# Kernel optimization log

Hardware: AMD Instinct MI355X
Metric: run time of the kernel (lower is better)

The kernel has to match this reference:

```python
import jax, jax.numpy as jnp
import numpy as np

H = 16  # n_heads

def setup_inputs() -> dict:
    key = jax.random.key(0)
    ks = jax.random.split(key, 11)
    B, L, D = 2, 2048, 1024
    w = 1.0 / np.sqrt(D).astype(np.float32)
    return {
        "query": jax.random.normal(ks[0], (B, L, D), jnp.float32),
        "key":   jax.random.normal(ks[1], (B, L, D), jnp.float32),
        "value": jax.random.normal(ks[2], (B, L, D), jnp.float32),
        "Wq": jax.random.normal(ks[3], (D, D), jnp.float32) * w,
        "bq": jax.random.normal(ks[4], (D,), jnp.float32) * 0.01,
        "Wk": jax.random.normal(ks[5], (D, D), jnp.float32) * w,
        "bk": jax.random.normal(ks[6], (D,), jnp.float32) * 0.01,
        "Wv": jax.random.normal(ks[7], (D, D), jnp.float32) * w,
        "bv": jax.random.normal(ks[8], (D,), jnp.float32) * 0.01,
        "Wo": jax.random.normal(ks[9], (D, D), jnp.float32) * w,
        "bo": jax.random.normal(ks[10], (D,), jnp.float32) * 0.01,
        "masksize": 256,
    }

def reference(query, key, value, Wq, bq, Wk, bk, Wv, bv, Wo, bo, masksize):
    B, L, D = query.shape
    d_k = D // H
    scale = 1.0 / np.sqrt(d_k).astype(np.float32)

    def proj(x, W, b):
        # nn.Linear: x @ W.T + b, then [B,L,H,d_k] -> [B,H,L,d_k]
        return (x @ W.T + b).reshape(B, L, H, d_k).transpose(0, 2, 1, 3)

    q = proj(query, Wq, bq)
    k = proj(key, Wk, bk)
    v = proj(value, Wv, bv)

    # Sliding-window float mask (faithful to original: a 0/1 FLOAT tensor is
    # passed as attn_mask to SDPA, so it is ADDED to scores, not -inf-masked).
    half = masksize // 2
    i = jnp.arange(L)[:, None]
    j = jnp.arange(L)[None, :]
    band = (jnp.abs(i - j) <= half).astype(q.dtype)  # [L, L]

    scores = jnp.einsum('bhqd,bhkd->bhqk', q, k) * scale + band  # [B,H,L,L]
    attn = jax.nn.softmax(scores, axis=-1)
    out = jnp.einsum('bhqk,bhkd->bhqd', attn, v)  # [B,H,L,d_k]
    out = out.transpose(0, 2, 1, 3).reshape(B, L, D)
    return out @ Wo.T + bo
```

## Files before the change

### kernel.cpp

```cpp
#include <hip/hip_runtime.h>
#include <hip/hip_bf16.h>

#define Hh 16
#define Ll 2048
#define Dd 1024
#define DK 64
#define Mm 4096
#define Kk 1024
#define Nn 1024

typedef short bf16x8 __attribute__((ext_vector_type(8)));
typedef float f32x4 __attribute__((ext_vector_type(4)));

static __device__ __forceinline__ unsigned short f2bf(float f) {
    union { __hip_bfloat16 b; unsigned short u; } cv;
    cv.b = __float2bfloat16(f);
    return cv.u;
}

static __device__ __forceinline__ unsigned packtr(float a, float b) {
    return __builtin_amdgcn_perm(__builtin_bit_cast(unsigned, b),
                                 __builtin_bit_cast(unsigned, a), 0x07060302u);
}

static __device__ __forceinline__ float fexp2(float x) {
    return __builtin_amdgcn_exp2f(x);
}

static __device__ __forceinline__ void glds16(const ushort* g, ushort* l) {
    __builtin_amdgcn_global_load_lds((const __attribute__((address_space(1))) unsigned int*)g,
                                     (__attribute__((address_space(3))) unsigned int*)l,
                                     16, 0, 0);
}

__global__ __launch_bounds__(256) void cast_all(
    const float* __restrict__ q, const float* __restrict__ k, const float* __restrict__ v,
    const float* __restrict__ wq, const float* __restrict__ wk, const float* __restrict__ wv,
    const float* __restrict__ wo,
    ushort* __restrict__ qb, ushort* __restrict__ kb, ushort* __restrict__ vb,
    ushort* __restrict__ wqb, ushort* __restrict__ wkb, ushort* __restrict__ wvb,
    ushort* __restrict__ wob) {
    const int bx = blockIdx.x;
    const float4* s; ushort4* d; int base;
    if      (bx <  4096) { s = (const float4*)q;  d = (ushort4*)qb;  base = 0; }
    else if (bx <  8192) { s = (const float4*)k;  d = (ushort4*)kb;  base = 4096; }
    else if (bx < 12288) { s = (const float4*)v;  d = (ushort4*)vb;  base = 8192; }
    else if (bx < 13312) { s = (const float4*)wq; d = (ushort4*)wqb; base = 12288; }
    else if (bx < 14336) { s = (const float4*)wk; d = (ushort4*)wkb; base = 13312; }
    else if (bx < 15360) { s = (const float4*)wv; d = (ushort4*)wvb; base = 14336; }
    else                 { s = (const float4*)wo; d = (ushort4*)wob; base = 15360; }
    const int i = (bx - base) * 256 + threadIdx.x;
    float4 vv = s[i];
    ushort4 o;
    o.x = f2bf(vv.x); o.y = f2bf(vv.y); o.z = f2bf(vv.z); o.w = f2bf(vv.w);
    d[i] = o;
}

__global__ __launch_bounds__(256) void gemm_qkv(
    const ushort* __restrict__ A0, const ushort* __restrict__ A1, const ushort* __restrict__ A2,
    const ushort* __restrict__ W0, const ushort* __restrict__ W1, const ushort* __restrict__ W2,
    const float* __restrict__ b0, const float* __restrict__ b1, const float* __restrict__ b2,
    ushort* __restrict__ O0, ushort* __restrict__ O1, ushort* __restrict__ OVt) {
    __shared__ __align__(16) ushort SM[2 * 128 * 32];
    ushort* As = SM;
    ushort* Bs = SM + 4096;

    const int fl = blockIdx.x;
    const int xcd = fl & 7, bcoli = (fl >> 3) & 7, slot = fl >> 6;
    const int g = slot * 8 + xcd;
    const int z = g >> 5;
    const int browi = g & 31;

    const ushort* A = (z == 0) ? A0 : (z == 1) ? A1 : A2;
    const ushort* W = (z == 0) ? W0 : (z == 1) ? W1 : W2;
    const float* bias = (z == 0) ? b0 : (z == 1) ? b1 : b2;

    const int t = threadIdx.x;
    const int wave = t >> 6, lane = t & 63;
    const int quad = lane >> 4, l15 = lane & 15;
    const int brow = browi * 128, bcol = bcoli * 128;
    const int wr = (wave >> 1) * 64, wc = (wave & 1) * 64;
    const int gr = wave * 16 + (lane >> 2);
    const int gc = (lane & 3) * 8;

    f32x4 acc[4][4] = {};

    for (int k0 = 0; k0 < Kk; k0 += 32) {
        __syncthreads();
        glds16(A + (size_t)(brow + gr) * Kk + k0 + gc,      As + wave * 512);
        glds16(A + (size_t)(brow + 64 + gr) * Kk + k0 + gc, As + 2048 + wave * 512);
        glds16(W + (size_t)(bcol + gr) * Kk + k0 + gc,      Bs + wave * 512);
        glds16(W + (size_t)(bcol + 64 + gr) * Kk + k0 + gc, Bs + 2048 + wave * 512);
        __syncthreads();

        bf16x8 af[4], bfr[4];
#pragma unroll
        for (int i = 0; i < 4; i++)
            af[i] = *(const bf16x8*)(As + (wr + i * 16 + l15) * 32 + quad * 8);
#pragma unroll
        for (int j = 0; j < 4; j++)
            bfr[j] = *(const bf16x8*)(Bs + (wc + j * 16 + l15) * 32 + quad * 8);
#pragma unroll
        for (int i = 0; i < 4; i++)
#pragma unroll
            for (int j = 0; j < 4; j++)
                acc[i][j] = __builtin_amdgcn_mfma_f32_16x16x32_bf16(af[i], bfr[j], acc[i][j], 0, 0, 0);
    }

    if (z < 2) {
        ushort* Out = (z == 0) ? O0 : O1;
        const float oscl = (z == 0) ? 0.18033688f : 1.0f;
        const int b = brow >> 11;
        const int lbase = (brow & 2047) + wr;
        const int h = (bcol + wc) >> 6;
        ushort* T = SM + wave * 1280;
        __syncthreads();
#pragma unroll
        for (int i = 0; i < 4; i++) {
#pragma unroll
            for (int j = 0; j < 4; j++) {
                const float bv = bias[bcol + wc + j * 16 + l15];
#pragma unroll
                for (int r = 0; r < 4; r++)
                    T[(quad * 4 + r) * 80 + j * 16 + l15] = f2bf((acc[i][j][r] + bv) * oscl);
            }
            const int r8 = lane >> 3, c8 = lane & 7;
#pragma unroll
            for (int pass = 0; pass < 2; pass++) {
                const uint4 val = *(const uint4*)(T + (pass * 8 + r8) * 80 + c8 * 8);
                const int l = lbase + i * 16 + pass * 8 + r8;
                *(uint4*)(Out + ((size_t)(b * Hh + h) * Ll + l) * DK + c8 * 8) = val;
            }
        }
    } else {
        ushort* T = SM;
        const int b = brow >> 11;
        const int lbase = brow & 2047;
        const int npr = (wave & 1) * 16 + l15;
#pragma unroll
        for (int j = 0; j < 4; j++) {
            __syncthreads();
            const float bv = bias[bcol + wc + j * 16 + l15];
#pragma unroll
            for (int i = 0; i < 4; i++)
#pragma unroll
                for (int r = 0; r < 4; r++) {
                    const int m = wr + i * 16 + quad * 4 + r;
                    T[npr * 136 + m] = f2bf(acc[i][j][r] + bv);
                }
            __syncthreads();
#pragma unroll
            for (int cc = 0; cc < 2; cc++) {
                const int idx = t + cc * 256;
                const int ni = idx >> 4;
                const int ms = idx & 15;
                const int n = bcol + (ni >> 4) * 64 + j * 16 + (ni & 15);
                const int hh = n >> 6, dk = n & 63;
                uint4 val = *(const uint4*)(T + ni * 136 + ms * 8);
                *(uint4*)(OVt + ((size_t)(b * Hh + hh) * DK + dk) * Ll + lbase + ms * 8) = val;
            }
        }
    }
}

__global__ __launch_bounds__(256, 2) void attn_kernel(const ushort* __restrict__ Q,
                                                      const ushort* __restrict__ Kp,
                                                      const ushort* __restrict__ Vt,
                                                      ushort* __restrict__ Oout,
                                                      const int* __restrict__ masksize) {
    __shared__ __align__(16) ushort SM[32768];
    const int t = threadIdx.x;
    const int wave = t >> 6, lane = t & 63;
    const int quad = lane >> 4, l15 = lane & 15;
    const int bx = blockIdx.x;
    const int bh = bx & 31, qc = bx >> 5;
    const int q0w = qc * 128 + wave * 32;
    const int half = masksize[0] >> 1;
    const unsigned wid = (unsigned)(2 * half);

    const ushort* Qb = Q + (size_t)bh * (Ll * DK);
    const ushort* Kb = Kp + (size_t)bh * (Ll * DK);
    const ushort* Vb = Vt + (size_t)bh * (DK * Ll);

    const bf16x8 qA0 = *(const bf16x8*)(Qb + (size_t)(q0w + l15) * DK + quad * 8);
    const bf16x8 qA1 = *(const bf16x8*)(Qb + (size_t)(q0w + l15) * DK + 32 + quad * 8);
    const bf16x8 qB0 = *(const bf16x8*)(Qb + (size_t)(q0w + 16 + l15) * DK + quad * 8);
    const bf16x8 qB1 = *(const bf16x8*)(Qb + (size_t)(q0w + 16 + l15) * DK + 32 + quad * 8);

    const float C2IN  = (1.0f - 24.0f) * 1.44269504088896f;
    const float C2OUT = -24.0f * 1.44269504088896f;
    const float E1 = 2.718281828f;

    bf16x8 onesf;
#pragma unroll
    for (int j = 0; j < 8; j++) onesf[j] = (short)0x3F80;

    f32x4 OA0[4] = {}, OB0[4] = {}, OA1[4] = {}, OB1[4] = {};
    f32x4 SA0 = {}, SB0 = {}, SA1 = {}, SB1 = {};

    const int krow = lane >> 2;
    const int kcol8 = (((lane & 3) ^ ((lane >> 3) & 3)) * 8);
    const int qsw8 = (quad ^ ((l15 >> 1) & 3)) * 8;
    const int vd8 = lane >> 3;
    const int vgp = 2 * (lane & 7);

#define STAGE_J(J, BUF)                                                                    \
    do {                                                                                   \
        const int kt0_ = (J) * 64, kt1_ = 1024 + (J) * 64;                                 \
        if (wave < 2) {                                                                    \
            const int ktk_ = (wave == 0) ? kt0_ : kt1_;                                    \
            ushort* dst_ = SM + wave * 8192 + (BUF) * 4096;                                \
            _Pragma("unroll")                                                              \
            for (int c_ = 0; c_ < 4; c_++)                                                 \
                _Pragma("unroll")                                                          \
                for (int pan_ = 0; pan_ < 2; pan_++)                                       \
                    glds16(Kb + (size_t)(ktk_ + c_ * 16 + krow) * DK + pan_ * 32 + kcol8,  \
                           dst_ + pan_ * 2048 + c_ * 512);                                 \
        } else {                                                                           \
            const int ktv_ = (wave == 2) ? kt0_ : kt1_;                                    \
            ushort* dst_ = SM + 16384 + (wave - 2) * 8192 + (BUF) * 4096;                  \
            _Pragma("unroll")                                                              \
            for (int s_ = 0; s_ < 8; s_++) {                                               \
                const int d_ = s_ * 8 + vd8;                                               \
                glds16(Vb + (size_t)d_ * Ll + ktv_ + ((vgp ^ (d_ & 14)) * 4),              \
                       dst_ + s_ * 512);                                                   \
            }                                                                              \
        }                                                                                  \
    } while (0)

#define STREAM_BODY(KB, VB, KT, CV, OAx, OBx, SAx, SBx, UNIF)                              \
    _Pragma("unroll")                                                                      \
    for (int s = 0; s < 2; s++) {                                                          \
        const bf16x8 kf00 = *(const bf16x8*)((KB) + ((2 * s) * 16 + l15) * 32 + qsw8);     \
        const bf16x8 kf01 = *(const bf16x8*)((KB) + 2048 + ((2 * s) * 16 + l15) * 32 + qsw8); \
        const bf16x8 kf10 = *(const bf16x8*)((KB) + ((2 * s + 1) * 16 + l15) * 32 + qsw8); \
        const bf16x8 kf11 = *(const bf16x8*)((KB) + 2048 + ((2 * s + 1) * 16 + l15) * 32 + qsw8); \
        f32x4 zA0 = __builtin_amdgcn_mfma_f32_16x16x32_bf16(kf00, qA0, (CV), 0, 0, 0);     \
        zA0 = __builtin_amdgcn_mfma_f32_16x16x32_bf16(kf01, qA1, zA0, 0, 0, 0);            \
        f32x4 zA1 = __builtin_amdgcn_mfma_f32_16x16x32_bf16(kf10, qA0, (CV), 0, 0, 0);     \
        zA1 = __builtin_amdgcn_mfma_f32_16x16x32_bf16(kf11, qA1, zA1, 0, 0, 0);            \
        f32x4 zB0 = __builtin_amdgcn_mfma_f32_16x16x32_bf16(kf00, qB0, (CV), 0, 0, 0);     \
        zB0 = __builtin_amdgcn_mfma_f32_16x16x32_bf16(kf01, qB1, zB0, 0, 0, 0);            \
        f32x4 zB1 = __builtin_amdgcn_mfma_f32_16x16x32_bf16(kf10, qB0, (CV), 0, 0, 0);     \
        zB1 = __builtin_amdgcn_mfma_f32_16x16x32_bf16(kf11, qB1, zB1, 0, 0, 0);            \
        float pA[8], pB[8];                                                                \
        if (UNIF) {                                                                        \
            _Pragma("unroll")                                                              \
            for (int g = 0; g < 2; g++)                                                    \
                _Pragma("unroll")                                                          \
                for (int r = 0; r < 4; r++) {                                              \
                    pA[g * 4 + r] = fexp2(g ? zA1[r] : zA0[r]);                            \
                    pB[g * 4 + r] = fexp2(g ? zB1[r] : zB0[r]);                            \
                }                                                                          \
        } else {                                                                           \
            const int kb = (KT) + s * 32 + quad * 4 + half;                                \
            _Pragma("unroll")                                                              \
            for (int g = 0; g < 2; g++)                                                    \
                _Pragma("unroll")                                                          \
                for (int r = 0; r < 4; r++) {                                              \
                    const unsigned ttA = (unsigned)(kb + g * 16 + r - (q0w + l15));        \
                    const unsigned ttB = (unsigned)(kb + g * 16 + r - (q0w + 16 + l15));   \
                    pA[g * 4 + r] = fexp2(g ? zA1[r] : zA0[r]) * (ttA <= wid ? E1 : 1.0f); \
                    pB[g * 4 + r] = fexp2(g ? zB1[r] : zB0[r]) * (ttB <= wid ? E1 : 1.0f); \
                }                                                                          \
        }                                                                                  \
        bf16x8 pfA, pfB;                                                                   \
        ((unsigned*)&pfA)[0] = packtr(pA[0], pA[1]);                                       \
        ((unsigned*)&pfA)[1] = packtr(pA[2], pA[3]);                                       \
        ((unsigned*)&pfA)[2] = packtr(pA[4], pA[5]);                                       \
        ((unsigned*)&pfA)[3] = packtr(pA[6], pA[7]);                                       \
        ((unsigned*)&pfB)[0] = packtr(pB[0], pB[1]);                                       \
        ((unsigned*)&pfB)[1] = packtr(pB[2], pB[3]);                                       \
        ((unsigned*)&pfB)[2] = packtr(pB[4], pB[5]);                                       \
        ((unsigned*)&pfB)[3] = packtr(pB[6], pB[7]);                                       \
        SAx = __builtin_amdgcn_mfma_f32_16x16x32_bf16(pfA, onesf, SAx, 0, 0, 0);           \
        SBx = __builtin_amdgcn_mfma_f32_16x16x32_bf16(pfB, onesf, SBx, 0, 0, 0);           \
        _Pragma("unroll")                                                                  \
        for (int i = 0; i < 4; i++) {                                                      \
            const int bi = (i * 16 + l15) * 64;                                            \
            const int x14 = l15 & 14;                                                      \
            const ushort4 v1 = *(const ushort4*)((VB) + bi + (((s * 8 + quad) ^ x14) * 4)); \
            const ushort4 v2 = *(const ushort4*)((VB) + bi + (((s * 8 + 4 + quad) ^ x14) * 4)); \
            bf16x8 vc;                                                                     \
            *(ushort4*)&vc = v1;                                                           \
            *((ushort4*)&vc + 1) = v2;                                                     \
            OAx[i] = __builtin_amdgcn_mfma_f32_16x16x32_bf16(pfA, vc, OAx[i], 0, 0, 0);    \
            OBx[i] = __builtin_amdgcn_mfma_f32_16x16x32_bf16(pfB, vc, OBx[i], 0, 0, 0);    \
        }                                                                                  \
    }

    STAGE_J(0, 0);
    int cur = 0;
    const int qlo = q0w, qhi = q0w + 31;

    for (int j = 0; j < 16; ++j) {
        const int kt0 = j * 64, kt1 = 1024 + j * 64;
        __syncthreads();
        if (j < 15) STAGE_J(j + 1, cur ^ 1);

        const ushort* K0b = SM + cur * 4096;
        const ushort* K1b = SM + 8192 + cur * 4096;
        const ushort* V0b = SM + 16384 + cur * 4096;
        const ushort* V1b = SM + 24576 + cur * 4096;

        const bool allout0 = (kt0 + 63 < qlo - half) || (kt0 > qhi + half);
        const bool allin0  = (kt0 >= qhi - half) && (kt0 + 63 <= qlo + half);
        const bool allout1 = (kt1 + 63 < qlo - half) || (kt1 > qhi + half);
        const bool allin1  = (kt1 >= qhi - half) && (kt1 + 63 <= qlo + half);

        if ((allin0 || allout0) && (allin1 || allout1)) {
            const float c0 = allin0 ? C2IN : C2OUT;
            const float c1 = allin1 ? C2IN : C2OUT;
            const f32x4 cv0 = {c0, c0, c0, c0};
            const f32x4 cv1 = {c1, c1, c1, c1};
            STREAM_BODY(K0b, V0b, kt0, cv0, OA0, OB0, SA0, SB0, 1);
            STREAM_BODY(K1b, V1b, kt1, cv1, OA1, OB1, SA1, SB1, 1);
        } else {
            const f32x4 cvo = {C2OUT, C2OUT, C2OUT, C2OUT};
            STREAM_BODY(K0b, V0b, kt0, cvo, OA0, OB0, SA0, SB0, 0);
            STREAM_BODY(K1b, V1b, kt1, cvo, OA1, OB1, SA1, SB1, 0);
        }
        cur ^= 1;
    }
#undef STAGE_J
#undef STREAM_BODY

    float liA[4], liB[4];
#pragma unroll
    for (int r = 0; r < 4; r++) {
        liA[r] = 1.0f / (SA0[r] + SA1[r]);
        liB[r] = 1.0f / (SB0[r] + SB1[r]);
    }

    const int b = bh >> 4, h = bh & 15;
#pragma unroll
    for (int i = 0; i < 4; i++)
#pragma unroll
        for (int r = 0; r < 4; r++) {
            const int qa = q0w + quad * 4 + r;
            Oout[((size_t)b * Ll + qa) * Dd + h * DK + i * 16 + l15] =
                f2bf((OA0[i][r] + OA1[i][r]) * liA[r]);
            Oout[((size_t)b * Ll + qa + 16) * Dd + h * DK + i * 16 + l15] =
                f2bf((OB0[i][r] + OB1[i][r]) * liB[r]);
        }
}

__global__ __launch_bounds__(256) void gemm_o(const ushort* __restrict__ A,
                                              const ushort* __restrict__ W,
                                              const float* __restrict__ bias,
                                              float* __restrict__ Out) {
    __shared__ __align__(16) ushort As[64 * 32];
    __shared__ __align__(16) ushort Bs[128 * 32];
    const int fl = blockIdx.x;
    const int xcd = fl & 7, bcoli = (fl >> 3) & 7, slot = fl >> 6;
    const int g = slot * 8 + xcd;
    const int t = threadIdx.x;
    const int wave = t >> 6, lane = t & 63;
    const int quad = lane >> 4, l15 = lane & 15;
    const int brow = g * 64, bcol = bcoli * 128;
    const int wr = (wave >> 1) * 32, wc = (wave & 1) * 64;
    const int gr = wave * 16 + (lane >> 2);
    const int gc = (lane & 3) * 8;

    f32x4 acc[2][4] = {};

    for (int k0 = 0; k0 < Kk; k0 += 32) {
        __syncthreads();
        glds16(A + (size_t)(brow + gr) * Kk + k0 + gc,      As + wave * 512);
        glds16(W + (size_t)(bcol + gr) * Kk + k0 + gc,      Bs + wave * 512);
        glds16(W + (size_t)(bcol + 64 + gr) * Kk + k0 + gc, Bs + 2048 + wave * 512);
        __syncthreads();

        bf16x8 af[2], bfr[4];
#pragma unroll
        for (int i = 0; i < 2; i++)
            af[i] = *(const bf16x8*)(As + (wr + i * 16 + l15) * 32 + quad * 8);
#pragma unroll
        for (int j = 0; j < 4; j++)
            bfr[j] = *(const bf16x8*)(Bs + (wc + j * 16 + l15) * 32 + quad * 8);
#pragma unroll
        for (int i = 0; i < 2; i++)
#pragma unroll
            for (int j = 0; j < 4; j++)
                acc[i][j] = __builtin_amdgcn_mfma_f32_16x16x32_bf16(af[i], bfr[j], acc[i][j], 0, 0, 0);
    }

#pragma unroll
    for (int i = 0; i < 2; i++)
#pragma unroll
        for (int j = 0; j < 4; j++) {
            const int n = bcol + wc + j * 16 + l15;
            const float bv = bias[n];
#pragma unroll
            for (int r = 0; r < 4; r++) {
                const int m = brow + wr + i * 16 + quad * 4 + r;
                Out[(size_t)m * Nn + n] = acc[i][j][r] + bv;
            }
        }
}

extern "C" void kernel_launch(void* const* d_in, const int* in_sizes, int n_in,
                              void* d_out, int out_size, void* d_ws, size_t ws_size,
                              hipStream_t stream) {
    const float* query = (const float*)d_in[0];
    const float* key   = (const float*)d_in[1];
    const float* value = (const float*)d_in[2];
    const float* Wq = (const float*)d_in[3];
    const float* bq = (const float*)d_in[4];
    const float* Wk = (const float*)d_in[5];
    const float* bk = (const float*)d_in[6];
    const float* Wv = (const float*)d_in[7];
    const float* bv = (const float*)d_in[8];
    const float* Wo = (const float*)d_in[9];
    const float* bo = (const float*)d_in[10];
    const int* masksize = (const int*)d_in[11];

    char* ws = (char*)d_ws;
    const size_t MB = 1024 * 1024;
    ushort* qb  = (ushort*)(ws + 0 * MB);
    ushort* kbf = (ushort*)(ws + 8 * MB);
    ushort* vbf = (ushort*)(ws + 16 * MB);
    ushort* wqb = (ushort*)(ws + 24 * MB);
    ushort* wkb = (ushort*)(ws + 26 * MB);
    ushort* wvb = (ushort*)(ws + 28 * MB);
    ushort* wob = (ushort*)(ws + 30 * MB);
    ushort* Qp  = (ushort*)(ws + 32 * MB);
    ushort* Kp  = (ushort*)(ws + 40 * MB);
    ushort* Vt  = (ushort*)(ws + 48 * MB);
    ushort* AO  = (ushort*)(ws + 56 * MB);

    cast_all<<<16384, 256, 0, stream>>>(query, key, value, Wq, Wk, Wv, Wo,
                                        qb, kbf, vbf, wqb, wkb, wvb, wob);

    gemm_qkv<<<768, 256, 0, stream>>>(qb, kbf, vbf,
                                      wqb, wkb, wvb,
                                      bq, bk, bv,
                                      Qp, Kp, Vt);

    attn_kernel<<<512, 256, 0, stream>>>(Qp, Kp, Vt, AO, masksize);

    gemm_o<<<512, 256, 0, stream>>>(AO, wob, bo, (float*)d_out);
}
```

Before: 219.1 us.

## Deepen GEMM K-tile to 64 with XOR-swizzled LDS and larger gemm_o tiles

Both projection GEMMs now stage a 64-wide K slice per iteration instead of 32, which halves the number of barrier pairs per block. Each row's 16-byte chunks are stored in LDS under an XOR swizzle so the fragment reads avoid bank conflicts. gemm_o moves from 64x128 to 128x128 tiles and launches half as many blocks, giving each block more MFMA work per loaded byte. The cost is more LDS and registers per block, and fewer blocks in gemm_o, which may lower occupancy.

Result: slower. 225.2 us (+2.8%).

```diff
diff --git a/kernel.cpp b/kernel.cpp
--- a/kernel.cpp
+++ b/kernel.cpp
@@ -61,9 +61,9 @@
     const ushort* __restrict__ W0, const ushort* __restrict__ W1, const ushort* __restrict__ W2,
     const float* __restrict__ b0, const float* __restrict__ b1, const float* __restrict__ b2,
     ushort* __restrict__ O0, ushort* __restrict__ O1, ushort* __restrict__ OVt) {
-    __shared__ __align__(16) ushort SM[2 * 128 * 32];
+    __shared__ __align__(16) ushort SM[2 * 128 * 64];
     ushort* As = SM;
-    ushort* Bs = SM + 4096;
+    ushort* Bs = SM + 8192;
 
     const int fl = blockIdx.x;
     const int xcd = fl & 7, bcoli = (fl >> 3) & 7, slot = fl >> 6;
@@ -80,31 +80,39 @@
     const int quad = lane >> 4, l15 = lane & 15;
     const int brow = browi * 128, bcol = bcoli * 128;
     const int wr = (wave >> 1) * 64, wc = (wave & 1) * 64;
-    const int gr = wave * 16 + (lane >> 2);
-    const int gc = (lane & 3) * 8;
+    const int sr = lane >> 3;
+    const int sg = ((lane & 7) ^ sr) * 8;
 
     f32x4 acc[4][4] = {};
 
-    for (int k0 = 0; k0 < Kk; k0 += 32) {
-        __syncthreads();
-        glds16(A + (size_t)(brow + gr) * Kk + k0 + gc,      As + wave * 512);
-        glds16(A + (size_t)(brow + 64 + gr) * Kk + k0 + gc, As + 2048 + wave * 512);
-        glds16(W + (size_t)(bcol + gr) * Kk + k0 + gc,      Bs + wave * 512);
-        glds16(W + (size_t)(bcol + 64 + gr) * Kk + k0 + gc, Bs + 2048 + wave * 512);
-        __syncthreads();
-
-        bf16x8 af[4], bfr[4];
-#pragma unroll
-        for (int i = 0; i < 4; i++)
-            af[i] = *(const bf16x8*)(As + (wr + i * 16 + l15) * 32 + quad * 8);
-#pragma unroll
-        for (int j = 0; j < 4; j++)
-            bfr[j] = *(const bf16x8*)(Bs + (wc + j * 16 + l15) * 32 + quad * 8);
-#pragma unroll
-        for (int i = 0; i < 4; i++)
+    for (int k0 = 0; k0 < Kk; k0 += 64) {
+        __syncthreads();
+#pragma unroll
+        for (int c = 0; c < 4; c++) {
+            const int row = wave * 32 + c * 8;
+            glds16(A + (size_t)(brow + row + sr) * Kk + k0 + sg, As + row * 64);
+            glds16(W + (size_t)(bcol + row + sr) * Kk + k0 + sg, Bs + row * 64);
+        }
+        __syncthreads();
+
+        bf16x8 af[2][4], bfr[2][4];
+#pragma unroll
+        for (int kk = 0; kk < 2; kk++) {
+            const int pos8 = (((kk * 4 + quad) ^ (l15 & 7)) * 8);
+#pragma unroll
+            for (int i = 0; i < 4; i++)
+                af[kk][i] = *(const bf16x8*)(As + (wr + i * 16 + l15) * 64 + pos8);
 #pragma unroll
             for (int j = 0; j < 4; j++)
-                acc[i][j] = __builtin_amdgcn_mfma_f32_16x16x32_bf16(af[i], bfr[j], acc[i][j], 0, 0, 0);
+                bfr[kk][j] = *(const bf16x8*)(Bs + (wc + j * 16 + l15) * 64 + pos8);
+        }
+#pragma unroll
+        for (int kk = 0; kk < 2; kk++)
+#pragma unroll
+            for (int i = 0; i < 4; i++)
+#pragma unroll
+                for (int j = 0; j < 4; j++)
+                    acc[i][j] = __builtin_amdgcn_mfma_f32_16x16x32_bf16(af[kk][i], bfr[kk][j], acc[i][j], 0, 0, 0);
     }
 
     if (z < 2) {
@@ -349,44 +357,54 @@
                                               const ushort* __restrict__ W,
                                               const float* __restrict__ bias,
                                               float* __restrict__ Out) {
-    __shared__ __align__(16) ushort As[64 * 32];
-    __shared__ __align__(16) ushort Bs[128 * 32];
+    __shared__ __align__(16) ushort SM[2 * 128 * 64];
+    ushort* As = SM;
+    ushort* Bs = SM + 8192;
     const int fl = blockIdx.x;
     const int xcd = fl & 7, bcoli = (fl >> 3) & 7, slot = fl >> 6;
-    const int g = slot * 8 + xcd;
+    const int browi = slot * 8 + xcd;
     const int t = threadIdx.x;
     const int wave = t >> 6, lane = t & 63;
     const int quad = lane >> 4, l15 = lane & 15;
-    const int brow = g * 64, bcol = bcoli * 128;
-    const int wr = (wave >> 1) * 32, wc = (wave & 1) * 64;
-    const int gr = wave * 16 + (lane >> 2);
-    const int gc = (lane & 3) * 8;
-
-    f32x4 acc[2][4] = {};
-
-    for (int k0 = 0; k0 < Kk; k0 += 32) {
-        __syncthreads();
-        glds16(A + (size_t)(brow + gr) * Kk + k0 + gc,      As + wave * 512);
-        glds16(W + (size_t)(bcol + gr) * Kk + k0 + gc,      Bs + wave * 512);
-        glds16(W + (size_t)(bcol + 64 + gr) * Kk + k0 + gc, Bs + 2048 + wave * 512);
-        __syncthreads();
-
-        bf16x8 af[2], bfr[4];
-#pragma unroll
-        for (int i = 0; i < 2; i++)
-            af[i] = *(const bf16x8*)(As + (wr + i * 16 + l15) * 32 + quad * 8);
-#pragma unroll
-        for (int j = 0; j < 4; j++)
-            bfr[j] = *(const bf16x8*)(Bs + (wc + j * 16 + l15) * 32 + quad * 8);
-#pragma unroll
-        for (int i = 0; i < 2; i++)
+    const int brow = browi * 128, bcol = bcoli * 128;
+    const int wr = (wave >> 1) * 64, wc = (wave & 1) * 64;
+    const int sr = lane >> 3;
+    const int sg = ((lane & 7) ^ sr) * 8;
+
+    f32x4 acc[4][4] = {};
+
+    for (int k0 = 0; k0 < Kk; k0 += 64) {
+        __syncthreads();
+#pragma unroll
+        for (int c = 0; c < 4; c++) {
+            const int row = wave * 32 + c * 8;
+            glds16(A + (size_t)(brow + row + sr) * Kk + k0 + sg, As + row * 64);
+            glds16(W + (size_t)(bcol + row + sr) * Kk + k0 + sg, Bs + row * 64);
+        }
+        __syncthreads();
+
+        bf16x8 af[2][4], bfr[2][4];
+#pragma unroll
+        for (int kk = 0; kk < 2; kk++) {
+            const int pos8 = (((kk * 4 + quad) ^ (l15 & 7)) * 8);
+#pragma unroll
+            for (int i = 0; i < 4; i++)
+                af[kk][i] = *(const bf16x8*)(As + (wr + i * 16 + l15) * 64 + pos8);
 #pragma unroll
             for (int j = 0; j < 4; j++)
-                acc[i][j] = __builtin_amdgcn_mfma_f32_16x16x32_bf16(af[i], bfr[j], acc[i][j], 0, 0, 0);
-    }
-
-#pragma unroll
-    for (int i = 0; i < 2; i++)
+                bfr[kk][j] = *(const bf16x8*)(Bs + (wc + j * 16 + l15) * 64 + pos8);
+        }
+#pragma unroll
+        for (int kk = 0; kk < 2; kk++)
+#pragma unroll
+            for (int i = 0; i < 4; i++)
+#pragma unroll
+                for (int j = 0; j < 4; j++)
+                    acc[i][j] = __builtin_amdgcn_mfma_f32_16x16x32_bf16(af[kk][i], bfr[kk][j], acc[i][j], 0, 0, 0);
+    }
+
+#pragma unroll
+    for (int i = 0; i < 4; i++)
 #pragma unroll
         for (int j = 0; j < 4; j++) {
             const int n = bcol + wc + j * 16 + l15;
@@ -439,5 +457,5 @@
 
     attn_kernel<<<512, 256, 0, stream>>>(Qp, Kp, Vt, AO, masksize);
 
-    gemm_o<<<512, 256, 0, stream>>>(AO, wob, bo, (float*)d_out);
-}
+    gemm_o<<<256, 256, 0, stream>>>(AO, wob, bo, (float*)d_out);
+}
```
